# Kernel optimization log

Measured on AMD Instinct MI355X. Metric: run time of the kernel, lower is better.

## Reference

```python
import jax, jax.numpy as jnp
import numpy as np

B, NF, HS, S = 4, 5, 512, 1024  # batch, face strips, face side dims (L=9, S=2*HS)


def _wrap_prev(region, x, j, i, w, rev=False):
    # neighbour on previous face strip, wrapping face 0 -> face 4
    vm = x[:, :4, j, i]
    vw = x[:, 4, j, i]
    if rev:
        vm = jnp.flip(vm, -1)
        vw = jnp.flip(vw, -1)
    return jnp.concatenate([(vw - region[:, 0])[:, None] * w,
                            (vm - region[:, 1:]) * w], axis=1)


def _wrap_next(region, x, j, i, w, rev=False):
    # neighbour on next face strip, wrapping face 4 -> face 0
    vm = x[:, 1:, j, i]
    vw = x[:, 0, j, i]
    if rev:
        vm = jnp.flip(vm, -1)
        vw = jnp.flip(vw, -1)
    return jnp.concatenate([(vm - region[:, :4]) * w,
                            (vw - region[:, 4])[:, None] * w], axis=1)


def _gradient(x, poles, wi, we, wcn, wne, wnne, wnw, wnww, wwe, wsw, wsse, wse, wcs):
    Bx, Fx, HS, S = x.shape
    out = jnp.zeros((Bx, 4, Fx, HS, S), x.dtype)

    def put(o, rows, cols, comps):
        return o.at[:, :, :, rows, cols].set(jnp.stack(comps, axis=1))

    # inner grid
    ii = x[:, :, 1:HS-1, 1:S-1]
    comps = [
        (x[:, :, :HS-2, :S-2] - ii) * wi[0],
        (x[:, :, 2:HS, 2:S] - ii) * wi[1],
        (x[:, :, :HS-2, 1:S-1] - ii) * wi[2] + (x[:, :, 1:HS-1, 2:S] - ii) * wi[3],
        (x[:, :, 1:HS-1, :S-2] - ii) * wi[4] + (x[:, :, 2:HS, 1:S-1] - ii) * wi[5],
    ]
    out = put(out, slice(1, HS-1), slice(1, S-1), comps)

    # east edge
    ei = x[:, :, 0, 1:HS]
    comps = [
        _wrap_prev(ei, x, HS-1, slice(HS, S-1), we[0]),
        (x[:, :, 1, 2:HS+1] - ei) * we[1],
        _wrap_prev(ei, x, HS-1, slice(HS+1, S), we[2]) + (x[:, :, 0, 2:HS+1] - ei) * we[3],
        (x[:, :, 0, 0:HS-1] - ei) * we[4] + (x[:, :, 1, 1:HS] - ei) * we[5],
    ]
    out = put(out, 0, slice(1, HS), comps)

    # cn corner
    ci = x[:, :, 0, HS]
    comps = [
        _wrap_prev(ci, x, HS-1, S-1, wcn[0]),
        (x[:, :, 1, HS+1] - ci) * wcn[1],
        (x[:, :, 0, HS+1] - ci) * wcn[2],
        (x[:, :, 0, HS-1] - ci) * wcn[3] + (x[:, :, 1, HS] - ci) * wcn[4],
    ]
    out = put(out, 0, HS, comps)

    # ne edge
    ni = x[:, :, 0, HS+1:S-1]
    comps = [
        _wrap_prev(ni, x, slice(1, HS-1), S-1, wne[0], rev=True) + _wrap_prev(ni, x, slice(2, HS), S-1, wne[1], rev=True),
        (x[:, :, 1, HS+2:S] - ni) * wne[2] + (x[:, :, 1, HS+1:S-1] - ni) * wne[3],
        (x[:, :, 0, HS+2:S] - ni) * wne[4],
        (x[:, :, 0, HS:S-2] - ni) * wne[5],
    ]
    out = put(out, 0, slice(HS+1, S-1), comps)

    # nne corner (north pole neighbour)
    qi = x[:, :, 0, S-1]
    comps = [
        _wrap_prev(qi, x, 0, S-1, wnne[0]) + _wrap_prev(qi, x, 1, S-1, wnne[1]),
        _wrap_next(qi, x, 0, S-1, wnne[2]) + (x[:, :, 1, S-1] - qi) * wnne[3],
        (poles[:, 1] - qi) * wnne[4],
        (x[:, :, 0, S-2] - qi) * wnne[5],
    ]
    out = put(out, 0, S-1, comps)

    # nw edge
    vi = x[:, :, 1:HS-1, S-1]
    comps = [
        (x[:, :, 0:HS-2, S-2] - vi) * wnw[0],
        _wrap_next(vi, x, 0, slice(HS+1, S-1), wnw[1], rev=True),
        (x[:, :, 0:HS-2, S-1] - vi) * wnw[2] + _wrap_next(vi, x, 0, slice(HS+2, S), wnw[3], rev=True),
        (x[:, :, 1:HS-1, S-2] - vi) * wnw[4] + (x[:, :, 2:HS, S-1] - vi) * wnw[5],
    ]
    out = put(out, slice(1, HS-1), S-1, comps)

    # nww corner
    gi = x[:, :, HS-1, S-1]
    comps = [
        (x[:, :, HS-2, S-2] - gi) * wnww[0],
        _wrap_next(gi, x, 0, HS, wnww[1]),
        (x[:, :, HS-2, S-1] - gi) * wnww[2] + _wrap_next(gi, x, 0, HS+1, wnww[3]),
        (x[:, :, HS-1, S-2] - gi) * wnww[4] + _wrap_next(gi, x, 0, HS-1, wnww[5]),
    ]
    out = put(out, HS-1, S-1, comps)

    # west edge
    ui = x[:, :, HS-1, HS:S-1]
    comps = [
        (x[:, :, HS-2, HS-1:S-2] - ui) * wwe[0],
        _wrap_next(ui, x, 0, slice(1, HS), wwe[1]),
        (x[:, :, HS-2, HS:S-1] - ui) * wwe[2] + (x[:, :, HS-1, HS+1:S] - ui) * wwe[3],
        (x[:, :, HS-1, HS-1:S-2] - ui) * wwe[4] + _wrap_next(ui, x, 0, slice(0, HS-1), wwe[5]),
    ]
    out = put(out, HS-1, slice(HS, S-1), comps)

    # sw edge
    si = x[:, :, HS-1, 1:HS]
    comps = [
        (x[:, :, HS-2, 0:HS-1] - si) * wsw[0],
        _wrap_next(si, x, slice(0, HS-1), 0, wsw[1], rev=True),
        (x[:, :, HS-2, 1:HS] - si) * wsw[2] + (x[:, :, HS-1, 2:HS+1] - si) * wsw[3],
        (x[:, :, HS-1, 0:HS-1] - si) * wsw[4] + _wrap_next(si, x, slice(1, HS), 0, wsw[5], rev=True),
    ]
    out = put(out, HS-1, slice(1, HS), comps)

    # sse corner (south pole neighbour)
    pi = x[:, :, HS-1, 0]
    comps = [
        _wrap_prev(pi, x, HS-1, 0, wsse[0]),
        _wrap_next(pi, x, HS-1, 0, wsse[1]),
        (x[:, :, HS-2, 0] - pi) * wsse[2] + (x[:, :, HS-1, 1] - pi) * wsse[3],
        (poles[:, 0] - pi) * wsse[4],
    ]
    out = put(out, HS-1, 0, comps)

    # se edge
    ri = x[:, :, 1:HS-1, 0]
    comps = [
        _wrap_prev(ri, x, HS-1, slice(2, HS), wse[0], rev=True) + _wrap_prev(ri, x, HS-1, slice(1, HS-1), wse[1], rev=True),
        (x[:, :, 1:HS-1, 1] - ri) * wse[2] + (x[:, :, 2:HS, 1] - ri) * wse[3],
        (x[:, :, 0:HS-2, 0] - ri) * wse[4],
        (x[:, :, 2:HS, 0] - ri) * wse[5],
    ]
    out = put(out, slice(1, HS-1), 0, comps)

    # cs corner
    di = x[:, :, 0, 0]
    comps = [
        _wrap_prev(di, x, HS-1, HS-1, wcs[0]),
        (x[:, :, 1, 1] - di) * wcs[1],
        _wrap_prev(di, x, HS-1, HS, wcs[2]) + (x[:, :, 0, 1] - di) * wcs[3],
        (x[:, :, 1, 0] - di) * wcs[4],
    ]
    out = put(out, 0, 0, comps)
    return out


def setup_inputs() -> dict:
    key = jax.random.key(0)
    ks = jax.random.split(key, 14)
    rn = lambda k, s: jax.random.normal(k, s, dtype=jnp.float32)
    return {
        "x": rn(ks[0], (B, NF, HS, S)),
        "poles": rn(ks[1], (B, 2, 1)),
        "w_inner": rn(ks[2], (6, HS-2, S-2)),
        "w_east": rn(ks[3], (6, HS-1)),
        "w_cn": rn(ks[4], (5,)),
        "w_ne": rn(ks[5], (6, HS-2)),
        "w_nne": rn(ks[6], (6,)),
        "w_nw": rn(ks[7], (6, HS-2)),
        "w_nww": rn(ks[8], (6,)),
        "w_west": rn(ks[9], (6, HS-1)),
        "w_sw": rn(ks[10], (6, HS-1)),
        "w_sse": rn(ks[11], (5,)),
        "w_se": rn(ks[12], (6, HS-2)),
        "w_cs": rn(ks[13], (5,)),
    }


def reference(x, poles, w_inner, w_east, w_cn, w_ne, w_nne, w_nw, w_nww, w_west, w_sw, w_sse, w_se, w_cs):
    # output: [B, 4, 5, HS, S] weighted neighbour-difference stencil components
    return _gradient(x, poles, w_inner, w_east, w_cn, w_ne, w_nne, w_nw, w_nww,
                     w_west, w_sw, w_sse, w_se, w_cs)
```

## Files before the change

### kernel.cpp

```cpp
#include <hip/hip_runtime.h>
#include <hip/hip_bf16.h>

#define Bc  4
#define NFc 5
#define HSc 512
#define Sc  1024

#define X(ff,jj,ii) x[xb + ((size_t)(ff)*HSc + (size_t)(jj))*Sc + (size_t)(ii)]
#define LW(arr,k,stride,m) (arr)[(k)*(stride)+(m)]

__global__ __launch_bounds__(256) void icograd_kernel(
    const float* __restrict__ x,    const float* __restrict__ poles,
    const float* __restrict__ wi,   const float* __restrict__ we,
    const float* __restrict__ wcn,  const float* __restrict__ wne,
    const float* __restrict__ wnne, const float* __restrict__ wnw,
    const float* __restrict__ wnww, const float* __restrict__ wwe,
    const float* __restrict__ wsw,  const float* __restrict__ wsse,
    const float* __restrict__ wse,  const float* __restrict__ wcs,
    float* __restrict__ out)
{
    const int i  = blockIdx.x * blockDim.x + threadIdx.x;
    const int j  = blockIdx.y;
    const int bf = blockIdx.z;
    const int b  = bf / NFc;
    const int f  = bf % NFc;

    const size_t xb = (size_t)b * (NFc * HSc * Sc);
    const float  cc = X(f, j, i);
    const int fp = (f == 0) ? 4 : f - 1;
    const int fn = (f == 4) ? 0 : f + 1;

    float c0, c1, c2, c3;

    if (j > 0 && j < HSc - 1) {
        if (i > 0 && i < Sc - 1) {
            const int wb = (j - 1) * (Sc - 2) + (i - 1);
            const int ws = (HSc - 2) * (Sc - 2);
            const float w0 = wi[wb];
            const float w1 = wi[wb + ws];
            const float w2 = wi[wb + 2 * ws];
            const float w3 = wi[wb + 3 * ws];
            const float w4 = wi[wb + 4 * ws];
            const float w5 = wi[wb + 5 * ws];
            c0 = (X(f, j - 1, i - 1) - cc) * w0;
            c1 = (X(f, j + 1, i + 1) - cc) * w1;
            c2 = (X(f, j - 1, i)     - cc) * w2 + (X(f, j,     i + 1) - cc) * w3;
            c3 = (X(f, j,     i - 1) - cc) * w4 + (X(f, j + 1, i)     - cc) * w5;
        } else if (i == 0) {
            const int m = j - 1;
            c0 = (X(fp, HSc - 1, 511 - m) - cc) * LW(wse, 0, 510, m)
               + (X(fp, HSc - 1, 510 - m) - cc) * LW(wse, 1, 510, m);
            c1 = (X(f, j,     1) - cc) * LW(wse, 2, 510, m)
               + (X(f, j + 1, 1) - cc) * LW(wse, 3, 510, m);
            c2 = (X(f, j - 1, 0) - cc) * LW(wse, 4, 510, m);
            c3 = (X(f, j + 1, 0) - cc) * LW(wse, 5, 510, m);
        } else {
            const int m = j - 1;
            c0 = (X(f, j - 1, Sc - 2) - cc) * LW(wnw, 0, 510, m);
            c1 = (X(fn, 0, Sc - 2 - m) - cc) * LW(wnw, 1, 510, m);
            c2 = (X(f, j - 1, Sc - 1) - cc) * LW(wnw, 2, 510, m)
               + (X(fn, 0, Sc - 1 - m) - cc) * LW(wnw, 3, 510, m);
            c3 = (X(f, j,     Sc - 2) - cc) * LW(wnw, 4, 510, m)
               + (X(f, j + 1, Sc - 1) - cc) * LW(wnw, 5, 510, m);
        }
    } else if (j == 0) {
        if (i == 0) {
            c0 = (X(fp, HSc - 1, HSc - 1) - cc) * LW(wcs, 0, 1, 0);
            c1 = (X(f, 1, 1) - cc) * LW(wcs, 1, 1, 0);
            c2 = (X(fp, HSc - 1, HSc) - cc) * LW(wcs, 2, 1, 0)
               + (X(f, 0, 1) - cc) * LW(wcs, 3, 1, 0);
            c3 = (X(f, 1, 0) - cc) * LW(wcs, 4, 1, 0);
        } else if (i <= HSc - 1) {
            const int m = i - 1;
            c0 = (X(fp, HSc - 1, HSc + m) - cc) * LW(we, 0, 511, m);
            c1 = (X(f, 1, i + 1) - cc) * LW(we, 1, 511, m);
            c2 = (X(fp, HSc - 1, HSc + 1 + m) - cc) * LW(we, 2, 511, m)
               + (X(f, 0, i + 1) - cc) * LW(we, 3, 511, m);
            c3 = (X(f, 0, i - 1) - cc) * LW(we, 4, 511, m)
               + (X(f, 1, i)     - cc) * LW(we, 5, 511, m);
        } else if (i == HSc) {
            c0 = (X(fp, HSc - 1, Sc - 1) - cc) * LW(wcn, 0, 1, 0);
            c1 = (X(f, 1, HSc + 1) - cc) * LW(wcn, 1, 1, 0);
            c2 = (X(f, 0, HSc + 1) - cc) * LW(wcn, 2, 1, 0);
            c3 = (X(f, 0, HSc - 1) - cc) * LW(wcn, 3, 1, 0)
               + (X(f, 1, HSc)     - cc) * LW(wcn, 4, 1, 0);
        } else if (i < Sc - 1) {
            const int m = i - (HSc + 1);
            c0 = (X(fp, 510 - m, Sc - 1) - cc) * LW(wne, 0, 510, m)
               + (X(fp, 511 - m, Sc - 1) - cc) * LW(wne, 1, 510, m);
            c1 = (X(f, 1, i + 1) - cc) * LW(wne, 2, 510, m)
               + (X(f, 1, i)     - cc) * LW(wne, 3, 510, m);
            c2 = (X(f, 0, i + 1) - cc) * LW(wne, 4, 510, m);
            c3 = (X(f, 0, i - 1) - cc) * LW(wne, 5, 510, m);
        } else {
            const float p1 = poles[b * 2 + 1];
            c0 = (X(fp, 0, Sc - 1) - cc) * LW(wnne, 0, 1, 0)
               + (X(fp, 1, Sc - 1) - cc) * LW(wnne, 1, 1, 0);
            c1 = (X(fn, 0, Sc - 1) - cc) * LW(wnne, 2, 1, 0)
               + (X(f,  1, Sc - 1) - cc) * LW(wnne, 3, 1, 0);
            c2 = (p1 - cc) * LW(wnne, 4, 1, 0);
            c3 = (X(f, 0, Sc - 2) - cc) * LW(wnne, 5, 1, 0);
        }
    } else {
        if (i == 0) {
            const float p0 = poles[b * 2 + 0];
            c0 = (X(fp, HSc - 1, 0) - cc) * LW(wsse, 0, 1, 0);
            c1 = (X(fn, HSc - 1, 0) - cc) * LW(wsse, 1, 1, 0);
            c2 = (X(f, HSc - 2, 0) - cc) * LW(wsse, 2, 1, 0)
               + (X(f, HSc - 1, 1) - cc) * LW(wsse, 3, 1, 0);
            c3 = (p0 - cc) * LW(wsse, 4, 1, 0);
        } else if (i <= HSc - 1) {
            const int m = i - 1;
            c0 = (X(f, HSc - 2, i - 1) - cc) * LW(wsw, 0, 511, m);
            c1 = (X(fn, 510 - m, 0) - cc) * LW(wsw, 1, 511, m);
            c2 = (X(f, HSc - 2, i)     - cc) * LW(wsw, 2, 511, m)
               + (X(f, HSc - 1, i + 1) - cc) * LW(wsw, 3, 511, m);
            c3 = (X(f, HSc - 1, i - 1) - cc) * LW(wsw, 4, 511, m)
               + (X(fn, 511 - m, 0)    - cc) * LW(wsw, 5, 511, m);
        } else if (i < Sc - 1) {
            const int m = i - HSc;
            c0 = (X(f, HSc - 2, i - 1) - cc) * LW(wwe, 0, 511, m);
            c1 = (X(fn, 0, 1 + m) - cc) * LW(wwe, 1, 511, m);
            c2 = (X(f, HSc - 2, i)     - cc) * LW(wwe, 2, 511, m)
               + (X(f, HSc - 1, i + 1) - cc) * LW(wwe, 3, 511, m);
            c3 = (X(f, HSc - 1, i - 1) - cc) * LW(wwe, 4, 511, m)
               + (X(fn, 0, m)          - cc) * LW(wwe, 5, 511, m);
        } else {
            c0 = (X(f, HSc - 2, Sc - 2) - cc) * LW(wnww, 0, 1, 0);
            c1 = (X(fn, 0, HSc) - cc) * LW(wnww, 1, 1, 0);
            c2 = (X(f, HSc - 2, Sc - 1) - cc) * LW(wnww, 2, 1, 0)
               + (X(fn, 0, HSc + 1)     - cc) * LW(wnww, 3, 1, 0);
            c3 = (X(f, HSc - 1, Sc - 2) - cc) * LW(wnww, 4, 1, 0)
               + (X(fn, 0, HSc - 1)     - cc) * LW(wnww, 5, 1, 0);
        }
    }

    const size_t cs = (size_t)NFc * HSc * Sc;
    const size_t ob = ((size_t)b * 4 * NFc + f) * (HSc * Sc)
                    + (size_t)j * Sc + (size_t)i;
    out[ob]          = c0;
    out[ob + cs]     = c1;
    out[ob + 2 * cs] = c2;
    out[ob + 3 * cs] = c3;
}

extern "C" void kernel_launch(void* const* d_in, const int* in_sizes, int n_in,
                              void* d_out, int out_size, void* d_ws, size_t ws_size,
                              hipStream_t stream) {
    const float* x    = (const float*)d_in[0];
    const float* pl   = (const float*)d_in[1];
    const float* wi   = (const float*)d_in[2];
    const float* we   = (const float*)d_in[3];
    const float* wcn  = (const float*)d_in[4];
    const float* wne  = (const float*)d_in[5];
    const float* wnne = (const float*)d_in[6];
    const float* wnw  = (const float*)d_in[7];
    const float* wnww = (const float*)d_in[8];
    const float* wwe  = (const float*)d_in[9];
    const float* wsw  = (const float*)d_in[10];
    const float* wsse = (const float*)d_in[11];
    const float* wse  = (const float*)d_in[12];
    const float* wcs  = (const float*)d_in[13];
    float* out = (float*)d_out;

    dim3 block(256, 1, 1);
    dim3 grid(Sc / 256, HSc, Bc * NFc);
    icograd_kernel<<<grid, block, 0, stream>>>(x, pl, wi, we, wcn, wne, wnne, wnw,
                                               wnww, wwe, wsw, wsse, wse, wcs, out);
}
```

Before: 262.0 us.

## Split into vectorized bulk-row kernel and separate boundary-row kernel

New measurement: 262.0 us. No clear change (-0.0%).

```diff
diff --git a/kernel.cpp b/kernel.cpp
--- a/kernel.cpp
+++ b/kernel.cpp
@@ -1,26 +1,169 @@
 #include <hip/hip_runtime.h>
-#include <hip/hip_bf16.h>
 
 #define Bc  4
 #define NFc 5
 #define HSc 512
 #define Sc  1024
+#define WSr (Sc - 2)
+#define WSp ((HSc - 2) * WSr)
+
+typedef float f4 __attribute__((ext_vector_type(4)));
+
+static __device__ __forceinline__ f4 load4u(const float* p) {
+    f4 r;
+    __builtin_memcpy(&r, p, 16);
+    return r;
+}
+
+static __device__ __forceinline__ void inner_scalar(
+    const float* __restrict__ xf, const float* __restrict__ wi,
+    int j, int i, float cc, float* c)
+{
+    const size_t wb = (size_t)(j - 1) * WSr + (i - 1);
+    const float w0 = wi[wb];
+    const float w1 = wi[wb + WSp];
+    const float w2 = wi[wb + 2 * (size_t)WSp];
+    const float w3 = wi[wb + 3 * (size_t)WSp];
+    const float w4 = wi[wb + 4 * (size_t)WSp];
+    const float w5 = wi[wb + 5 * (size_t)WSp];
+    c[0] = (xf[(size_t)(j - 1) * Sc + (i - 1)] - cc) * w0;
+    c[1] = (xf[(size_t)(j + 1) * Sc + (i + 1)] - cc) * w1;
+    c[2] = (xf[(size_t)(j - 1) * Sc + i] - cc) * w2
+         + (xf[(size_t)j * Sc + (i + 1)] - cc) * w3;
+    c[3] = (xf[(size_t)j * Sc + (i - 1)] - cc) * w4
+         + (xf[(size_t)(j + 1) * Sc + i] - cc) * w5;
+}
+
+__global__ __launch_bounds__(256) void icograd_bulk(
+    const float* __restrict__ x, const float* __restrict__ wi,
+    const float* __restrict__ wnw, const float* __restrict__ wse,
+    float* __restrict__ out)
+{
+    const int t  = threadIdx.x;
+    const int j  = blockIdx.x + 1;
+    const int bf = blockIdx.y;
+    const int b  = bf / NFc;
+    const int f  = bf % NFc;
+
+    const size_t xb = (size_t)b * (NFc * HSc * Sc);
+    const float* xf = x + xb + (size_t)f * (HSc * Sc);
+    const float* rm = xf + (size_t)(j - 1) * Sc;
+    const float* rc = xf + (size_t)j * Sc;
+    const float* rp = xf + (size_t)(j + 1) * Sc;
+    const int i0 = t * 4;
+
+    float c0[4], c1[4], c2[4], c3[4];
+
+    if (t >= 1 && t <= 254) {
+        const f4 xm = *(const f4*)(rm + i0);
+        const f4 xc = *(const f4*)(rc + i0);
+        const f4 xp = *(const f4*)(rp + i0);
+        const float xml = rm[i0 - 1];
+        const float xcl = rc[i0 - 1];
+        const float xcr = rc[i0 + 4];
+        const float xpr = rp[i0 + 4];
+
+        const float* wrow = wi + (size_t)(j - 1) * WSr + (i0 - 1);
+        const f4 w0 = load4u(wrow);
+        const f4 w1 = load4u(wrow + (size_t)WSp);
+        const f4 w2 = load4u(wrow + 2 * (size_t)WSp);
+        const f4 w3 = load4u(wrow + 3 * (size_t)WSp);
+        const f4 w4 = load4u(wrow + 4 * (size_t)WSp);
+        const f4 w5 = load4u(wrow + 5 * (size_t)WSp);
+
+        const float am1[4] = {xml, xm.x, xm.y, xm.z};
+        const float acm[4] = {xcl, xc.x, xc.y, xc.z};
+        const float acp[4] = {xc.y, xc.z, xc.w, xcr};
+        const float app[4] = {xp.y, xp.z, xp.w, xpr};
+        const float xcv[4] = {xc.x, xc.y, xc.z, xc.w};
+        const float xmv[4] = {xm.x, xm.y, xm.z, xm.w};
+        const float xpv[4] = {xp.x, xp.y, xp.z, xp.w};
+        const float w0v[4] = {w0.x, w0.y, w0.z, w0.w};
+        const float w1v[4] = {w1.x, w1.y, w1.z, w1.w};
+        const float w2v[4] = {w2.x, w2.y, w2.z, w2.w};
+        const float w3v[4] = {w3.x, w3.y, w3.z, w3.w};
+        const float w4v[4] = {w4.x, w4.y, w4.z, w4.w};
+        const float w5v[4] = {w5.x, w5.y, w5.z, w5.w};
+
+#pragma unroll
+        for (int e = 0; e < 4; ++e) {
+            const float cc = xcv[e];
+            c0[e] = (am1[e] - cc) * w0v[e];
+            c1[e] = (app[e] - cc) * w1v[e];
+            c2[e] = (xmv[e] - cc) * w2v[e] + (acp[e] - cc) * w3v[e];
+            c3[e] = (acm[e] - cc) * w4v[e] + (xpv[e] - cc) * w5v[e];
+        }
+    } else if (t == 0) {
+        {
+            const int m = j - 1;
+            const int fp = (f == 0) ? 4 : f - 1;
+            const float* xq = x + xb + (size_t)fp * (HSc * Sc);
+            const float cc = rc[0];
+            float cw[4];
+            cw[0] = (xq[(size_t)(HSc - 1) * Sc + (511 - m)] - cc) * wse[0 * 510 + m]
+                  + (xq[(size_t)(HSc - 1) * Sc + (510 - m)] - cc) * wse[1 * 510 + m];
+            cw[1] = (rc[1] - cc) * wse[2 * 510 + m]
+                  + (rp[1] - cc) * wse[3 * 510 + m];
+            cw[2] = (rm[0] - cc) * wse[4 * 510 + m];
+            cw[3] = (rp[0] - cc) * wse[5 * 510 + m];
+            c0[0] = cw[0]; c1[0] = cw[1]; c2[0] = cw[2]; c3[0] = cw[3];
+        }
+#pragma unroll
+        for (int e = 1; e < 4; ++e) {
+            float cw[4];
+            inner_scalar(xf, wi, j, e, rc[e], cw);
+            c0[e] = cw[0]; c1[e] = cw[1]; c2[e] = cw[2]; c3[e] = cw[3];
+        }
+    } else {
+#pragma unroll
+        for (int e = 0; e < 3; ++e) {
+            const int i = 1020 + e;
+            float cw[4];
+            inner_scalar(xf, wi, j, i, rc[i], cw);
+            c0[e] = cw[0]; c1[e] = cw[1]; c2[e] = cw[2]; c3[e] = cw[3];
+        }
+        {
+            const int m = j - 1;
+            const int fn = (f == 4) ? 0 : f + 1;
+            const float* xq = x + xb + (size_t)fn * (HSc * Sc);
+            const float cc = rc[Sc - 1];
+            float cw[4];
+            cw[0] = (rm[Sc - 2] - cc) * wnw[0 * 510 + m];
+            cw[1] = (xq[Sc - 2 - m] - cc) * wnw[1 * 510 + m];
+            cw[2] = (rm[Sc - 1] - cc) * wnw[2 * 510 + m]
+                  + (xq[Sc - 1 - m] - cc) * wnw[3 * 510 + m];
+            cw[3] = (rc[Sc - 2] - cc) * wnw[4 * 510 + m]
+                  + (rp[Sc - 1] - cc) * wnw[5 * 510 + m];
+            c0[3] = cw[0]; c1[3] = cw[1]; c2[3] = cw[2]; c3[3] = cw[3];
+        }
+    }
+
+    const size_t cs = (size_t)NFc * HSc * Sc;
+    float* ob = out + ((size_t)b * (4 * NFc) + f) * (HSc * Sc)
+                    + (size_t)j * Sc + i0;
+    f4 o0 = {c0[0], c0[1], c0[2], c0[3]};
+    f4 o1 = {c1[0], c1[1], c1[2], c1[3]};
+    f4 o2 = {c2[0], c2[1], c2[2], c2[3]};
+    f4 o3 = {c3[0], c3[1], c3[2], c3[3]};
+    *(f4*)(ob)          = o0;
+    *(f4*)(ob + cs)     = o1;
+    *(f4*)(ob + 2 * cs) = o2;
+    *(f4*)(ob + 3 * cs) = o3;
+}
 
 #define X(ff,jj,ii) x[xb + ((size_t)(ff)*HSc + (size_t)(jj))*Sc + (size_t)(ii)]
 #define LW(arr,k,stride,m) (arr)[(k)*(stride)+(m)]
 
-__global__ __launch_bounds__(256) void icograd_kernel(
+__global__ __launch_bounds__(256) void icograd_edge(
     const float* __restrict__ x,    const float* __restrict__ poles,
-    const float* __restrict__ wi,   const float* __restrict__ we,
-    const float* __restrict__ wcn,  const float* __restrict__ wne,
-    const float* __restrict__ wnne, const float* __restrict__ wnw,
+    const float* __restrict__ we,   const float* __restrict__ wcn,
+    const float* __restrict__ wne,  const float* __restrict__ wnne,
     const float* __restrict__ wnww, const float* __restrict__ wwe,
     const float* __restrict__ wsw,  const float* __restrict__ wsse,
-    const float* __restrict__ wse,  const float* __restrict__ wcs,
-    float* __restrict__ out)
+    const float* __restrict__ wcs,  float* __restrict__ out)
 {
     const int i  = blockIdx.x * blockDim.x + threadIdx.x;
-    const int j  = blockIdx.y;
+    const int j  = blockIdx.y ? (HSc - 1) : 0;
     const int bf = blockIdx.z;
     const int b  = bf / NFc;
     const int f  = bf % NFc;
@@ -32,44 +175,12 @@
 
     float c0, c1, c2, c3;
 
-    if (j > 0 && j < HSc - 1) {
-        if (i > 0 && i < Sc - 1) {
-            const int wb = (j - 1) * (Sc - 2) + (i - 1);
-            const int ws = (HSc - 2) * (Sc - 2);
-            const float w0 = wi[wb];
-            const float w1 = wi[wb + ws];
-            const float w2 = wi[wb + 2 * ws];
-            const float w3 = wi[wb + 3 * ws];
-            const float w4 = wi[wb + 4 * ws];
-            const float w5 = wi[wb + 5 * ws];
-            c0 = (X(f, j - 1, i - 1) - cc) * w0;
-            c1 = (X(f, j + 1, i + 1) - cc) * w1;
-            c2 = (X(f, j - 1, i)     - cc) * w2 + (X(f, j,     i + 1) - cc) * w3;
-            c3 = (X(f, j,     i - 1) - cc) * w4 + (X(f, j + 1, i)     - cc) * w5;
-        } else if (i == 0) {
-            const int m = j - 1;
-            c0 = (X(fp, HSc - 1, 511 - m) - cc) * LW(wse, 0, 510, m)
-               + (X(fp, HSc - 1, 510 - m) - cc) * LW(wse, 1, 510, m);
-            c1 = (X(f, j,     1) - cc) * LW(wse, 2, 510, m)
-               + (X(f, j + 1, 1) - cc) * LW(wse, 3, 510, m);
-            c2 = (X(f, j - 1, 0) - cc) * LW(wse, 4, 510, m);
-            c3 = (X(f, j + 1, 0) - cc) * LW(wse, 5, 510, m);
-        } else {
-            const int m = j - 1;
-            c0 = (X(f, j - 1, Sc - 2) - cc) * LW(wnw, 0, 510, m);
-            c1 = (X(fn, 0, Sc - 2 - m) - cc) * LW(wnw, 1, 510, m);
-            c2 = (X(f, j - 1, Sc - 1) - cc) * LW(wnw, 2, 510, m)
-               + (X(fn, 0, Sc - 1 - m) - cc) * LW(wnw, 3, 510, m);
-            c3 = (X(f, j,     Sc - 2) - cc) * LW(wnw, 4, 510, m)
-               + (X(f, j + 1, Sc - 1) - cc) * LW(wnw, 5, 510, m);
-        }
-    } else if (j == 0) {
+    if (j == 0) {
         if (i == 0) {
-            c0 = (X(fp, HSc - 1, HSc - 1) - cc) * LW(wcs, 0, 1, 0);
-            c1 = (X(f, 1, 1) - cc) * LW(wcs, 1, 1, 0);
-            c2 = (X(fp, HSc - 1, HSc) - cc) * LW(wcs, 2, 1, 0)
-               + (X(f, 0, 1) - cc) * LW(wcs, 3, 1, 0);
-            c3 = (X(f, 1, 0) - cc) * LW(wcs, 4, 1, 0);
+            c0 = (X(fp, HSc - 1, HSc - 1) - cc) * wcs[0];
+            c1 = (X(f, 1, 1) - cc) * wcs[1];
+            c2 = (X(fp, HSc - 1, HSc) - cc) * wcs[2] + (X(f, 0, 1) - cc) * wcs[3];
+            c3 = (X(f, 1, 0) - cc) * wcs[4];
         } else if (i <= HSc - 1) {
             const int m = i - 1;
             c0 = (X(fp, HSc - 1, HSc + m) - cc) * LW(we, 0, 511, m);
@@ -79,11 +190,10 @@
             c3 = (X(f, 0, i - 1) - cc) * LW(we, 4, 511, m)
                + (X(f, 1, i)     - cc) * LW(we, 5, 511, m);
         } else if (i == HSc) {
-            c0 = (X(fp, HSc - 1, Sc - 1) - cc) * LW(wcn, 0, 1, 0);
-            c1 = (X(f, 1, HSc + 1) - cc) * LW(wcn, 1, 1, 0);
-            c2 = (X(f, 0, HSc + 1) - cc) * LW(wcn, 2, 1, 0);
-            c3 = (X(f, 0, HSc - 1) - cc) * LW(wcn, 3, 1, 0)
-               + (X(f, 1, HSc)     - cc) * LW(wcn, 4, 1, 0);
+            c0 = (X(fp, HSc - 1, Sc - 1) - cc) * wcn[0];
+            c1 = (X(f, 1, HSc + 1) - cc) * wcn[1];
+            c2 = (X(f, 0, HSc + 1) - cc) * wcn[2];
+            c3 = (X(f, 0, HSc - 1) - cc) * wcn[3] + (X(f, 1, HSc) - cc) * wcn[4];
         } else if (i < Sc - 1) {
             const int m = i - (HSc + 1);
             c0 = (X(fp, 510 - m, Sc - 1) - cc) * LW(wne, 0, 510, m)
@@ -94,21 +204,21 @@
             c3 = (X(f, 0, i - 1) - cc) * LW(wne, 5, 510, m);
         } else {
             const float p1 = poles[b * 2 + 1];
-            c0 = (X(fp, 0, Sc - 1) - cc) * LW(wnne, 0, 1, 0)
-               + (X(fp, 1, Sc - 1) - cc) * LW(wnne, 1, 1, 0);
-            c1 = (X(fn, 0, Sc - 1) - cc) * LW(wnne, 2, 1, 0)
-               + (X(f,  1, Sc - 1) - cc) * LW(wnne, 3, 1, 0);
-            c2 = (p1 - cc) * LW(wnne, 4, 1, 0);
-            c3 = (X(f, 0, Sc - 2) - cc) * LW(wnne, 5, 1, 0);
+            c0 = (X(fp, 0, Sc - 1) - cc) * wnne[0]
+               + (X(fp, 1, Sc - 1) - cc) * wnne[1];
+            c1 = (X(fn, 0, Sc - 1) - cc) * wnne[2]
+               + (X(f,  1, Sc - 1) - cc) * wnne[3];
+            c2 = (p1 - cc) * wnne[4];
+            c3 = (X(f, 0, Sc - 2) - cc) * wnne[5];
         }
     } else {
         if (i == 0) {
             const float p0 = poles[b * 2 + 0];
-            c0 = (X(fp, HSc - 1, 0) - cc) * LW(wsse, 0, 1, 0);
-            c1 = (X(fn, HSc - 1, 0) - cc) * LW(wsse, 1, 1, 0);
-            c2 = (X(f, HSc - 2, 0) - cc) * LW(wsse, 2, 1, 0)
-               + (X(f, HSc - 1, 1) - cc) * LW(wsse, 3, 1, 0);
-            c3 = (p0 - cc) * LW(wsse, 4, 1, 0);
+            c0 = (X(fp, HSc - 1, 0) - cc) * wsse[0];
+            c1 = (X(fn, HSc - 1, 0) - cc) * wsse[1];
+            c2 = (X(f, HSc - 2, 0) - cc) * wsse[2]
+               + (X(f, HSc - 1, 1) - cc) * wsse[3];
+            c3 = (p0 - cc) * wsse[4];
         } else if (i <= HSc - 1) {
             const int m = i - 1;
             c0 = (X(f, HSc - 2, i - 1) - cc) * LW(wsw, 0, 511, m);
@@ -126,17 +236,17 @@
             c3 = (X(f, HSc - 1, i - 1) - cc) * LW(wwe, 4, 511, m)
                + (X(fn, 0, m)          - cc) * LW(wwe, 5, 511, m);
         } else {
-            c0 = (X(f, HSc - 2, Sc - 2) - cc) * LW(wnww, 0, 1, 0);
-            c1 = (X(fn, 0, HSc) - cc) * LW(wnww, 1, 1, 0);
-            c2 = (X(f, HSc - 2, Sc - 1) - cc) * LW(wnww, 2, 1, 0)
-               + (X(fn, 0, HSc + 1)     - cc) * LW(wnww, 3, 1, 0);
-            c3 = (X(f, HSc - 1, Sc - 2) - cc) * LW(wnww, 4, 1, 0)
-               + (X(fn, 0, HSc - 1)     - cc) * LW(wnww, 5, 1, 0);
+            c0 = (X(f, HSc - 2, Sc - 2) - cc) * wnww[0];
+            c1 = (X(fn, 0, HSc) - cc) * wnww[1];
+            c2 = (X(f, HSc - 2, Sc - 1) - cc) * wnww[2]
+               + (X(fn, 0, HSc + 1)     - cc) * wnww[3];
+            c3 = (X(f, HSc - 1, Sc - 2) - cc) * wnww[4]
+               + (X(fn, 0, HSc - 1)     - cc) * wnww[5];
         }
     }
 
     const size_t cs = (size_t)NFc * HSc * Sc;
-    const size_t ob = ((size_t)b * 4 * NFc + f) * (HSc * Sc)
+    const size_t ob = ((size_t)b * (4 * NFc) + f) * (HSc * Sc)
                     + (size_t)j * Sc + (size_t)i;
     out[ob]          = c0;
     out[ob + cs]     = c1;
@@ -163,8 +273,8 @@
     const float* wcs  = (const float*)d_in[13];
     float* out = (float*)d_out;
 
-    dim3 block(256, 1, 1);
-    dim3 grid(Sc / 256, HSc, Bc * NFc);
-    icograd_kernel<<<grid, block, 0, stream>>>(x, pl, wi, we, wcn, wne, wnne, wnw,
-                                               wnww, wwe, wsw, wsse, wse, wcs, out);
-}
+    icograd_bulk<<<dim3(HSc - 2, Bc * NFc, 1), dim3(256, 1, 1), 0, stream>>>(
+        x, wi, wnw, wse, out);
+    icograd_edge<<<dim3(Sc / 256, 2, Bc * NFc), dim3(256, 1, 1), 0, stream>>>(
+        x, pl, we, wcn, wne, wnne, wnww, wwe, wsw, wsse, wcs, out);
+}
```
